# Kernel optimization log

Hardware: AMD Instinct MI355X
Metric: run time of the kernel (lower is better)

## Reference

```python
import jax, jax.numpy as jnp
import numpy as np

H, D, K, FF = 8, 512, 64, 64  # n_head, feature_dim, key_feature_dim, dim_feedforward
L, B = 512, 32
LN_EPS = 1e-5


def _l2norm(x, eps=1e-12):
    # torch F.normalize: x / max(||x||, eps)
    n = jnp.sqrt(jnp.sum(x * x, axis=-1, keepdims=True))
    return x / jnp.maximum(n, eps)


def _layernorm(x, g, b, eps=LN_EPS):
    m = jnp.mean(x, axis=-1, keepdims=True)
    v = jnp.mean((x - m) ** 2, axis=-1, keepdims=True)
    return (x - m) * jax.lax.rsqrt(v + eps) * g + b


def setup_inputs() -> dict:
    key0 = jax.random.key(0)
    ks = jax.random.split(key0, 13)
    n = jax.random.normal
    s_kq = float(np.sqrt(2.0 / K))
    s_v = float(np.sqrt(2.0 / D))
    return {
        "query": n(ks[0], (L, B, D), jnp.float32),
        "key": n(ks[1], (L, B, D), jnp.float32),
        "value": n(ks[2], (L, B, D), jnp.float32),
        "WK": n(ks[3], (H, K, D), jnp.float32) * s_kq,
        "WQ": n(ks[4], (H, K, D), jnp.float32) * s_kq,
        "WV": n(ks[5], (H, D, D), jnp.float32) * s_v,
        "Wt": n(ks[6], (H, D, D), jnp.float32) * 0.04,  # trans_conv (default kaiming-ish scale)
        "W1": n(ks[7], (H, FF, D), jnp.float32) * 0.04,
        "b1": jnp.zeros((H, FF), jnp.float32),
        "W2": n(ks[8], (H, D, FF), jnp.float32) * 0.1,
        "b2": jnp.zeros((H, D), jnp.float32),
        "ln_g": jnp.ones((H, D), jnp.float32),
        "ln_b": jnp.zeros((H, D), jnp.float32),
    }


def reference(query, key, value, WK, WQ, WV, Wt, W1, b1, W2, b2, ln_g, ln_b):
    # query/key/value: [L, B, D]; per-head weights stacked on leading H axis.
    Lq, Bb, Dd = query.shape
    Hh = WK.shape[0]

    # per-head cosine-normalized Q/K projections: [H, B, L, K]
    wq = _l2norm(jnp.einsum('lbd,hkd->hblk', query, WQ))
    wk = _l2norm(jnp.einsum('lbd,hkd->hblk', key, WK))

    # attention scores [H, B, Lq, Lk], temp = 1
    dot = jnp.einsum('hbqc,hbkc->hbqk', wq, wk)
    aff = jax.nn.softmax(dot, axis=-1)
    # custom renorm: divide by column sums over the QUERY axis
    aff = aff / (1e-9 + jnp.sum(aff, axis=2, keepdims=True))

    wv = jnp.einsum('lbd,hed->hble', value, WV)        # [H, B, Lk, D]
    out = jnp.einsum('hbqk,hbke->hbqe', aff, wv)       # [H, B, Lq, D]
    out = jnp.transpose(out, (0, 2, 1, 3))             # [H, L, B, D]

    # residual-style trans_conv(query - out) -> relu
    o = jax.nn.relu(jnp.einsum('hlbd,hed->hlbe', query[None] - out, Wt))

    # TransNonlinear FFN (dropout = identity at eval)
    hff = jax.nn.relu(jnp.einsum('hlbd,hfd->hlbf', o, W1) + b1[:, None, None, :])
    s2 = jnp.einsum('hlbf,hdf->hlbd', hff, W2) + b2[:, None, None, :]
    x = _layernorm(o + s2, ln_g[:, None, None, :], ln_b[:, None, None, :])

    # concat heads on last dim, head 0 first: [L, B, H*D]
    return jnp.transpose(x, (1, 2, 0, 3)).reshape(Lq, Bb, Hh * Dd)
```

## Files before the change

### kernel.cpp

```cpp
#include <hip/hip_runtime.h>
#include <stdint.h>

#define HH 8
#define DDIM 512
#define KHEAD 64
#define FFD 64
#define LLEN 512
#define BBATCH 32
#define NTOK 16384

typedef unsigned short u16;
typedef __attribute__((ext_vector_type(8))) __bf16 bf16x8;
typedef __attribute__((ext_vector_type(4))) float f32x4;

__device__ __forceinline__ float bf2f(u16 u) {
    union { uint32_t i; float f; } v; v.i = ((uint32_t)u) << 16; return v.f;
}
__device__ __forceinline__ u16 f2bf(float f) {
    union { uint32_t i; float f; } v; v.f = f;
    return (u16)((v.i + 0x7FFFu + ((v.i >> 16) & 1u)) >> 16);
}

__device__ __forceinline__ void gload16(const void* g, void* l) {
    __builtin_amdgcn_global_load_lds(
        (const __attribute__((address_space(1))) void*)g,
        (__attribute__((address_space(3))) void*)l, 16, 0, 0);
}

struct ConvJob { const float* s; u16* d; int n4; };
struct ConvJobs { ConvJob j[6]; int nj; };

__global__ __launch_bounds__(256) void conv_multi(ConvJobs jobs) {
    for (int k = 0; k < jobs.nj; ++k) {
        const float* s = jobs.j[k].s;
        u16* d = jobs.j[k].d;
        const int n4 = jobs.j[k].n4;
        for (long i = (long)blockIdx.x * 256 + threadIdx.x; i < n4;
             i += (long)gridDim.x * 256) {
            float4 v = ((const float4*)s)[i];
            ushort4 o;
            o.x = f2bf(v.x); o.y = f2bf(v.y); o.z = f2bf(v.z); o.w = f2bf(v.w);
            ((ushort4*)d)[i] = o;
        }
    }
}

enum { M_PLAIN = 0, M_WQK = 1, M_SUBAUX = 2, M_RELU = 3, M_ADDAUX = 4, M_SCALECOL = 5 };

template<int BM, int BN, int MODE, int ZMAP, int SWAPXY>
__global__ __launch_bounds__(256) void mgemm(
    const u16* __restrict__ A, const u16* __restrict__ B, u16* __restrict__ C,
    int Kd, int lda, int ldb, int ldc,
    long Ash, long Asb, long Bsh, long Bsb, long Csh, long Csb, int nB2,
    const float* __restrict__ bias, int biasN,
    const void* __restrict__ auxp, long auxsh, long auxsb, int auxld)
{
    constexpr int WC = (BN == 128) ? 2 : 1;
    constexpr int WR = 4 / WC;
    constexpr int WTM = BM / WR;
    constexpr int WTN = BN / WC;
    constexpr int MF = WTM / 16;
    constexpr int NF = WTN / 16;
    constexpr int NCA = (BM * 64) / 4096;
    constexpr int NCB = (BN * 64) / 4096;
    __shared__ u16 As[2][BM * 32];
    __shared__ u16 Bs[2][BN * 32];

    const int z = blockIdx.z;
    int h2, b2;
    if (ZMAP == 0)      { h2 = z / nB2;      b2 = z % nB2; }
    else if (ZMAP == 1) { h2 = z & 7;        b2 = z >> 3; }
    else                { h2 = (z >> 3) & 7; b2 = ((z >> 6) << 3) | (z & 7); }
    const u16* Ab = A + h2 * Ash + b2 * Asb;
    const u16* Bb = B + h2 * Bsh + b2 * Bsb;
    const int bx = SWAPXY ? blockIdx.y : blockIdx.x;
    const int by = SWAPXY ? blockIdx.x : blockIdx.y;
    const int m0 = bx * BM, n0 = by * BN;
    const int t = threadIdx.x;
    const int lane = t & 63;
    const int w = t >> 6;
    const int wr = w / WC, wc = w % WC;
    const int tb = t * 16;
    const int wb = (t & 192) * 16;

    f32x4 acc[MF][NF];
    #pragma unroll
    for (int m = 0; m < MF; ++m)
        #pragma unroll
        for (int n = 0; n < NF; ++n)
            #pragma unroll
            for (int i = 0; i < 4; ++i) acc[m][n][i] = 0.f;

    const int ko = (lane >> 4) * 16;

    auto stage = [&](int buf, int k0) {
        #pragma unroll
        for (int c = 0; c < NCA; ++c) {
            const int byte = c * 4096 + tb;
            const int row = byte >> 6;
            gload16((const char*)(Ab + (long)(m0 + row) * lda + k0) + (byte & 63),
                    (char*)As[buf] + c * 4096 + wb);
        }
        #pragma unroll
        for (int c = 0; c < NCB; ++c) {
            const int byte = c * 4096 + tb;
            const int row = byte >> 6;
            gload16((const char*)(Bb + (long)(n0 + row) * ldb + k0) + (byte & 63),
                    (char*)Bs[buf] + c * 4096 + wb);
        }
    };

    stage(0, 0);
    __syncthreads();
    int cur = 0;
    const int nsteps = Kd >> 5;
    for (int s = 0; s < nsteps; ++s) {
        if (s + 1 < nsteps) stage(cur ^ 1, (s + 1) << 5);
        bf16x8 af[MF], bfr[NF];
        #pragma unroll
        for (int m = 0; m < MF; ++m)
            af[m] = *(const bf16x8*)((const char*)As[cur] + (wr * WTM + m * 16 + (lane & 15)) * 64 + ko);
        #pragma unroll
        for (int n = 0; n < NF; ++n)
            bfr[n] = *(const bf16x8*)((const char*)Bs[cur] + (wc * WTN + n * 16 + (lane & 15)) * 64 + ko);
        #pragma unroll
        for (int m = 0; m < MF; ++m)
            #pragma unroll
            for (int n = 0; n < NF; ++n)
                acc[m][n] = __builtin_amdgcn_mfma_f32_16x16x32_bf16(af[m], bfr[n], acc[m][n], 0, 0, 0);
        __syncthreads();
        cur ^= 1;
    }

    const int lr = (lane >> 4) * 4;
    const int lc = lane & 15;

    if constexpr (MODE == M_WQK) {
        const int h = (n0 + wc * WTN) >> 6;
        #pragma unroll
        for (int m = 0; m < MF; ++m) {
            #pragma unroll
            for (int i = 0; i < 4; ++i) {
                float s = 0.f;
                #pragma unroll
                for (int n = 0; n < NF; ++n) { const float v = acc[m][n][i]; s += v * v; }
                s += __shfl_xor(s, 1); s += __shfl_xor(s, 2);
                s += __shfl_xor(s, 4); s += __shfl_xor(s, 8);
                const float inv = 1.0f / fmaxf(sqrtf(s), 1e-12f);
                const int r = m0 + wr * WTM + m * 16 + lr + i;
                const int l = r >> 5, bq = r & 31;
                const int sw = (l & 7) << 3;
                u16* rowp = C + (((long)(h * BBATCH + bq) * LLEN + l) * KHEAD);
                #pragma unroll
                for (int n = 0; n < NF; ++n)
                    rowp[(lc + n * 16) ^ sw] = f2bf(acc[m][n][i] * inv);
            }
        }
    } else {
        const long cof = h2 * Csh + b2 * Csb;
        #pragma unroll
        for (int m = 0; m < MF; ++m) {
            #pragma unroll
            for (int i = 0; i < 4; ++i) {
                const int r = m0 + wr * WTM + m * 16 + lr + i;
                #pragma unroll
                for (int n = 0; n < NF; ++n) {
                    const int c = n0 + wc * WTN + n * 16 + lc;
                    float v = acc[m][n][i];
                    if (MODE == M_SUBAUX) {
                        const u16* q = (const u16*)auxp;
                        v = bf2f(q[auxsh * h2 + auxsb * b2 + (long)r * auxld + c]) - v;
                    } else if (MODE == M_RELU) {
                        if (bias) v += bias[h2 * biasN + c];
                        v = fmaxf(v, 0.0f);
                    } else if (MODE == M_ADDAUX) {
                        v += bias[h2 * biasN + c];
                        const u16* ax = (const u16*)auxp;
                        v += bf2f(ax[auxsh * h2 + auxsb * b2 + (long)r * auxld + c]);
                    } else if (MODE == M_SCALECOL) {
                        const float* cs = (const float*)auxp + auxsh * h2 + auxsb * b2;
                        v *= 1.0f / (1e-9f + cs[c]);
                    }
                    C[cof + (long)r * ldc + c] = f2bf(v);
                }
            }
        }
    }
}

__device__ __forceinline__ void xcd_decode(int wgid, int& qt, int& b, int& h) {
    const int r = wgid & 7;
    const int inner = wgid >> 3;
    qt = inner & 7;
    h = (inner >> 3) & 7;
    b = ((inner >> 6) << 3) | r;
}

__global__ __launch_bounds__(256) void attn_mfma(
    const u16* __restrict__ wq, const u16* __restrict__ wk,
    u16* __restrict__ P, float* __restrict__ colsum)
{
    __shared__ u16 qs[64 * 64];
    __shared__ u16 ks[512 * 64];
    __shared__ float smax[4][64];
    __shared__ float ssum[4][64];

    int qt, b, h;
    xcd_decode(blockIdx.x, qt, b, h);
    const long hb = h * BBATCH + b;
    const int t = threadIdx.x;
    const int lane = t & 63, w = t >> 6;
    const int wb = (t & 192) * 16;

    const char* qg = (const char*)(wq + (hb * LLEN + qt * 64) * KHEAD);
    const char* kg = (const char*)(wk + hb * LLEN * KHEAD);
    #pragma unroll
    for (int c = 0; c < 2; ++c)
        gload16(qg + c * 4096 + t * 16, (char*)qs + c * 4096 + wb);
    #pragma unroll
    for (int c = 0; c < 16; ++c)
        gload16(kg + c * 4096 + t * 16, (char*)ks + c * 4096 + wb);
    __syncthreads();

    const int l15 = lane & 15;
    const int g = lane >> 4;
    const int swz = (lane & 7) << 4;

    f32x4 acc[4][8];
    #pragma unroll
    for (int m = 0; m < 4; ++m)
        #pragma unroll
        for (int n = 0; n < 8; ++n)
            #pragma unroll
            for (int i = 0; i < 4; ++i) acc[m][n][i] = 0.f;

    #pragma unroll
    for (int kk = 0; kk < 2; ++kk) {
        bf16x8 af[4];
        #pragma unroll
        for (int m = 0; m < 4; ++m) {
            const int row = m * 16 + l15;
            af[m] = *(const bf16x8*)((const char*)qs + row * 128 + ((g * 16 + kk * 64) ^ swz));
        }
        #pragma unroll
        for (int n = 0; n < 8; ++n) {
            const int row = (w * 8 + n) * 16 + l15;
            const bf16x8 bfr = *(const bf16x8*)((const char*)ks + row * 128 + ((g * 16 + kk * 64) ^ swz));
            #pragma unroll
            for (int m = 0; m < 4; ++m)
                acc[m][n] = __builtin_amdgcn_mfma_f32_16x16x32_bf16(af[m], bfr, acc[m][n], 0, 0, 0);
        }
    }

    float rmax[4][4];
    #pragma unroll
    for (int m = 0; m < 4; ++m)
        #pragma unroll
        for (int i = 0; i < 4; ++i) {
            float mx = acc[m][0][i];
            #pragma unroll
            for (int n = 1; n < 8; ++n) mx = fmaxf(mx, acc[m][n][i]);
            mx = fmaxf(mx, __shfl_xor(mx, 1));
            mx = fmaxf(mx, __shfl_xor(mx, 2));
            mx = fmaxf(mx, __shfl_xor(mx, 4));
            mx = fmaxf(mx, __shfl_xor(mx, 8));
            if (l15 == 0) smax[w][m * 16 + g * 4 + i] = mx;
        }
    __syncthreads();
    #pragma unroll
    for (int m = 0; m < 4; ++m)
        #pragma unroll
        for (int i = 0; i < 4; ++i) {
            const int r = m * 16 + g * 4 + i;
            rmax[m][i] = fmaxf(fmaxf(smax[0][r], smax[1][r]),
                               fmaxf(smax[2][r], smax[3][r]));
        }
    float rinv[4][4];
    #pragma unroll
    for (int m = 0; m < 4; ++m)
        #pragma unroll
        for (int i = 0; i < 4; ++i) {
            float s = 0.f;
            #pragma unroll
            for (int n = 0; n < 8; ++n) {
                acc[m][n][i] = __expf(acc[m][n][i] - rmax[m][i]);
                s += acc[m][n][i];
            }
            s += __shfl_xor(s, 1); s += __shfl_xor(s, 2);
            s += __shfl_xor(s, 4); s += __shfl_xor(s, 8);
            if (l15 == 0) ssum[w][m * 16 + g * 4 + i] = s;
        }
    __syncthreads();
    #pragma unroll
    for (int m = 0; m < 4; ++m)
        #pragma unroll
        for (int i = 0; i < 4; ++i) {
            const int r = m * 16 + g * 4 + i;
            rinv[m][i] = 1.0f / (ssum[0][r] + ssum[1][r] + ssum[2][r] + ssum[3][r]);
        }

    u16* Pb = P + (hb * LLEN + qt * 64) * LLEN + w * 128;
    float cs[8];
    #pragma unroll
    for (int n = 0; n < 8; ++n) cs[n] = 0.f;
    #pragma unroll
    for (int m = 0; m < 4; ++m)
        #pragma unroll
        for (int i = 0; i < 4; ++i) {
            const int r = m * 16 + g * 4 + i;
            u16* pr = Pb + (long)r * LLEN + l15;
            const float iv = rinv[m][i];
            #pragma unroll
            for (int n = 0; n < 8; ++n) {
                const float p = acc[m][n][i] * iv;
                pr[n * 16] = f2bf(p);
                cs[n] += p;
            }
        }
    #pragma unroll
    for (int n = 0; n < 8; ++n) {
        cs[n] += __shfl_xor(cs[n], 16);
        cs[n] += __shfl_xor(cs[n], 32);
    }
    if (lane < 16) {
        float* cb = colsum + hb * 512 + w * 128 + lane;
        #pragma unroll
        for (int n = 0; n < 8; ++n) atomicAdd(&cb[n * 16], cs[n]);
    }
}

__global__ __launch_bounds__(256) void ffn2_ln(
    const u16* __restrict__ hff, const u16* __restrict__ W2bf,
    const float* __restrict__ b2, const u16* __restrict__ o,
    const float* __restrict__ lng, const float* __restrict__ lnb,
    float* __restrict__ out)
{
    __shared__ u16 W2s[512 * 64];
    __shared__ u16 hs[32 * 64];
    __shared__ float redS[4][32];
    __shared__ float redQ[4][32];

    const int h = blockIdx.z;
    const int m0 = blockIdx.x * 32;
    const int t = threadIdx.x;
    const int lane = t & 63, w = t >> 6;
    const int l15 = lane & 15, g = lane >> 4;
    const int wb = (t & 192) * 16;

    const char* w2g = (const char*)W2bf + (long)h * 65536;
    #pragma unroll
    for (int c = 0; c < 16; ++c) {
        const int idx = c * 4096 + t * 16;
        const int row = idx >> 7;
        const int g0 = (idx >> 4) & 7;
        gload16(w2g + row * 128 + ((g0 ^ (row & 7)) << 4),
                (char*)W2s + c * 4096 + wb);
    }
    {
        const int idx = t * 16;
        const int row = idx >> 7;
        const int g0 = (idx >> 4) & 7;
        gload16((const char*)(hff + ((long)h * NTOK + m0) * FFD) +
                    row * 128 + ((g0 ^ (row & 7)) << 4),
                (char*)hs + wb);
    }
    __syncthreads();

    f32x4 acc[2][8];
    #pragma unroll
    for (int m = 0; m < 2; ++m)
        #pragma unroll
        for (int n = 0; n < 8; ++n)
            #pragma unroll
            for (int i = 0; i < 4; ++i) acc[m][n][i] = 0.f;

    #pragma unroll
    for (int kk = 0; kk < 2; ++kk) {
        bf16x8 af[2];
        #pragma unroll
        for (int m = 0; m < 2; ++m) {
            const int row = m * 16 + l15;
            af[m] = *(const bf16x8*)((const char*)hs + row * 128 +
                                     (((kk * 4 + g) ^ (row & 7)) << 4));
        }
        #pragma unroll
        for (int n = 0; n < 8; ++n) {
            const int e = w * 128 + n * 16 + l15;
            const bf16x8 bfr = *(const bf16x8*)((const char*)W2s + e * 128 +
                                                (((kk * 4 + g) ^ (e & 7)) << 4));
            #pragma unroll
            for (int m = 0; m < 2; ++m)
                acc[m][n] = __builtin_amdgcn_mfma_f32_16x16x32_bf16(af[m], bfr, acc[m][n], 0, 0, 0);
        }
    }

    float b2v[8], gv[8], bv[8];
    #pragma unroll
    for (int n = 0; n < 8; ++n) {
        const int c = w * 128 + n * 16 + l15;
        b2v[n] = b2[h * DDIM + c];
        gv[n] = lng[h * DDIM + c];
        bv[n] = lnb[h * DDIM + c];
    }
    const u16* ob = o + ((long)h * NTOK + m0) * DDIM;
    #pragma unroll
    for (int m = 0; m < 2; ++m)
        #pragma unroll
        for (int i = 0; i < 4; ++i) {
            const int row = m * 16 + g * 4 + i;
            float s = 0.f, q = 0.f;
            #pragma unroll
            for (int n = 0; n < 8; ++n) {
                const int c = w * 128 + n * 16 + l15;
                const float v = acc[m][n][i] + b2v[n] + bf2f(ob[(long)row * DDIM + c]);
                acc[m][n][i] = v;
                s += v; q += v * v;
            }
            s += __shfl_xor(s, 1); q += __shfl_xor(q, 1);
            s += __shfl_xor(s, 2); q += __shfl_xor(q, 2);
            s += __shfl_xor(s, 4); q += __shfl_xor(q, 4);
            s += __shfl_xor(s, 8); q += __shfl_xor(q, 8);
            if (l15 == 0) { redS[w][row] = s; redQ[w][row] = q; }
        }
    __syncthreads();

    #pragma unroll
    for (int m = 0; m < 2; ++m)
        #pragma unroll
        for (int i = 0; i < 4; ++i) {
            const int row = m * 16 + g * 4 + i;
            const float s = redS[0][row] + redS[1][row] + redS[2][row] + redS[3][row];
            const float q = redQ[0][row] + redQ[1][row] + redQ[2][row] + redQ[3][row];
            const float mu = s * (1.0f / 512.0f);
            const float var = q * (1.0f / 512.0f) - mu * mu;
            const float rs = rsqrtf(var + 1e-5f);
            const int tok = m0 + row;
            const int b = tok >> 9, l = tok & 511;
            float* op = out + ((long)(l * BBATCH + b)) * (HH * DDIM) + h * DDIM;
            #pragma unroll
            for (int n = 0; n < 8; ++n) {
                const int c = w * 128 + n * 16 + l15;
                op[c] = (acc[m][n][i] - mu) * rs * gv[n] + bv[n];
            }
        }
}

extern "C" void kernel_launch(void* const* d_in, const int* in_sizes, int n_in,
                              void* d_out, int out_size, void* d_ws, size_t ws_size,
                              hipStream_t stream) {
    const float* query = (const float*)d_in[0];
    const float* key   = (const float*)d_in[1];
    const float* value = (const float*)d_in[2];
    const float* WK = (const float*)d_in[3];
    const float* WQ = (const float*)d_in[4];
    const float* WV = (const float*)d_in[5];
    const float* Wt = (const float*)d_in[6];
    const float* W1 = (const float*)d_in[7];
    const float* b1 = (const float*)d_in[8];
    const float* W2 = (const float*)d_in[9];
    const float* b2 = (const float*)d_in[10];
    const float* lng = (const float*)d_in[11];
    const float* lnb = (const float*)d_in[12];

    char* ws = (char*)d_ws;
    u16* kbf  = (u16*)(ws);
    u16* WQbf = (u16*)(ws + 16777216);
    u16* WKbf = (u16*)(ws + 17301504);
    u16* P    = (u16*)(ws);
    u16* vbf  = (u16*)(ws + 134217728);
    u16* WVbf = (u16*)(ws + 150994944);
    u16* o    = (u16*)(ws + 134217728);
    float* colsum = (float*)(ws + 268435456);
    u16* qbf  = (u16*)(ws + 268959744);
    u16* hff  = qbf;
    u16* wq   = (u16*)(ws + 285736960);
    u16* wk   = (u16*)(ws + 302514176);
    u16* Wtbf = (u16*)(ws + 285736960);
    u16* W1bf = (u16*)(ws + 289931264);
    u16* W2bf = (u16*)(ws + 290455552);
    u16* qmo = (u16*)d_out;
    u16* wvT = (u16*)((char*)d_out + 134217728);

    if (ws_size < 319291392u) return;

    hipMemsetAsync(colsum, 0, 524288, stream);
    const dim3 blk(256);

    {
        ConvJobs J;
        J.j[0] = { query, qbf, 2097152 };
        J.j[1] = { key,   kbf, 2097152 };
        J.j[2] = { value, vbf, 2097152 };
        J.j[3] = { WQ, WQbf, 65536 };
        J.j[4] = { WK, WKbf, 65536 };
        J.j[5] = { WV, WVbf, 524288 };
        J.nj = 6;
        conv_multi<<<dim3(2048), blk, 0, stream>>>(J);
    }

    mgemm<128, 128, M_WQK, 0, 1><<<dim3(4, 128, 1), blk, 0, stream>>>(
        qbf, WQbf, wq, 512, 512, 512, 0,
        0, 0, 0, 0, 0, 0, 1, nullptr, 0, nullptr, 0, 0, 0);
    mgemm<128, 128, M_WQK, 0, 1><<<dim3(4, 128, 1), blk, 0, stream>>>(
        kbf, WKbf, wk, 512, 512, 512, 0,
        0, 0, 0, 0, 0, 0, 1, nullptr, 0, nullptr, 0, 0, 0);

    attn_mfma<<<dim3(2048), blk, 0, stream>>>(wq, wk, P, colsum);

    {
        ConvJobs J;
        J.j[0] = { Wt, Wtbf, 524288 };
        J.j[1] = { W1, W1bf, 65536 };
        J.j[2] = { W2, W2bf, 65536 };
        J.nj = 3;
        conv_multi<<<dim3(1024), blk, 0, stream>>>(J);
    }

    mgemm<128, 128, M_SCALECOL, 2, 0><<<dim3(4, 4, 256), blk, 0, stream>>>(
        WVbf, vbf, wvT, 512, 512, BBATCH * DDIM, 512,
        (long)DDIM * DDIM, 0, 0, DDIM,
        (long)BBATCH * DDIM * LLEN, (long)DDIM * LLEN, 32,
        nullptr, 0, colsum, (long)BBATCH * 512, 512, 0);

    mgemm<128, 128, M_SUBAUX, 1, 0><<<dim3(4, 4, 256), blk, 0, stream>>>(
        P, wvT, qmo, 512, 512, 512, 512,
        (long)BBATCH * LLEN * LLEN, (long)LLEN * LLEN,
        (long)BBATCH * DDIM * LLEN, (long)DDIM * LLEN,
        (long)BBATCH * LLEN * DDIM, (long)LLEN * DDIM, 32,
        nullptr, 0, qbf, 0, DDIM, BBATCH * DDIM);

    mgemm<128, 128, M_RELU, 0, 1><<<dim3(4, 128, 8), blk, 0, stream>>>(
        qmo, Wtbf, o, 512, 512, 512, 512,
        (long)NTOK * DDIM, 0, (long)DDIM * DDIM, 0,
        (long)NTOK * DDIM, 0, 1, nullptr, 512, nullptr, 0, 0, 0);

    mgemm<128, 64, M_RELU, 0, 0><<<dim3(128, 1, 8), blk, 0, stream>>>(
        o, W1bf, hff, 512, 512, 512, 64,
        (long)NTOK * DDIM, 0, (long)FFD * DDIM, 0,
        (long)NTOK * FFD, 0, 1, b1, 64, nullptr, 0, 0, 0);

    ffn2_ln<<<dim3(512, 1, 8), blk, 0, stream>>>(hff, W2bf, b2, o, lng, lnb,
                                                 (float*)d_out);
}
```

Before: 766.2 us.

## Add 256x256-tile 512-thread GEMM kernel for the three large batched GEMMs

Result: faster. 746.4 us, median of 2 (-2.6%).

```diff
diff --git a/kernel.cpp b/kernel.cpp
--- a/kernel.cpp
+++ b/kernel.cpp
@@ -46,6 +46,138 @@
 }
 
 enum { M_PLAIN = 0, M_WQK = 1, M_SUBAUX = 2, M_RELU = 3, M_ADDAUX = 4, M_SCALECOL = 5 };
+
+template<int MODE, int ZMAP, int SWAPXY>
+__global__ __launch_bounds__(512) void mgemm256(
+    const u16* __restrict__ A, const u16* __restrict__ B, u16* __restrict__ C,
+    int Kd, int lda, int ldb, int ldc,
+    long Ash, long Asb, long Bsh, long Bsb, long Csh, long Csb, int nB2,
+    const float* __restrict__ bias, int biasN,
+    const void* __restrict__ auxp, long auxsh, long auxsb, int auxld)
+{
+    __shared__ u16 As[2][256 * 64];
+    __shared__ u16 Bs[2][256 * 64];
+
+    const int z = blockIdx.z;
+    int h2, b2;
+    if (ZMAP == 0)      { h2 = z / nB2;      b2 = z % nB2; }
+    else if (ZMAP == 1) { h2 = z & 7;        b2 = z >> 3; }
+    else                { h2 = (z >> 3) & 7; b2 = ((z >> 6) << 3) | (z & 7); }
+    const int bx = SWAPXY ? blockIdx.y : blockIdx.x;
+    const int by = SWAPXY ? blockIdx.x : blockIdx.y;
+    const int m0 = bx * 256, n0 = by * 256;
+    const u16* Ab = A + h2 * Ash + b2 * Asb + (long)m0 * lda;
+    const u16* Bb = B + h2 * Bsh + b2 * Bsb + (long)n0 * ldb;
+
+    const int t = threadIdx.x;
+    const int lane = t & 63;
+    const int w = t >> 6;
+    const int wm = w >> 2;
+    const int wn = w & 3;
+    const int l15 = lane & 15;
+    const int g = lane >> 4;
+
+    f32x4 acc[8][4];
+    #pragma unroll
+    for (int mf = 0; mf < 8; ++mf)
+        #pragma unroll
+        for (int nf = 0; nf < 4; ++nf)
+            #pragma unroll
+            for (int i = 0; i < 4; ++i) acc[mf][nf][i] = 0.f;
+
+    auto stageT = [&](int buf, int k0) {
+        #pragma unroll
+        for (int c = 0; c < 4; ++c) {
+            const int idx = c * 8192 + t * 16;
+            const int row = idx >> 7;
+            const int g0 = (idx >> 4) & 7;
+            gload16((const char*)(Ab + (long)row * lda + k0) + ((g0 ^ (row & 7)) << 4),
+                    (char*)As[buf] + c * 8192 + w * 1024);
+        }
+        #pragma unroll
+        for (int c = 0; c < 4; ++c) {
+            const int idx = c * 8192 + t * 16;
+            const int row = idx >> 7;
+            const int g0 = (idx >> 4) & 7;
+            gload16((const char*)(Bb + (long)row * ldb + k0) + ((g0 ^ (row & 7)) << 4),
+                    (char*)Bs[buf] + c * 8192 + w * 1024);
+        }
+    };
+
+    stageT(0, 0);
+    const int nt = Kd >> 6;
+    for (int T = 0; T < nt; ++T) {
+        asm volatile("s_waitcnt vmcnt(0)" ::: "memory");
+        __builtin_amdgcn_sched_barrier(0);
+        __builtin_amdgcn_s_barrier();
+        __builtin_amdgcn_sched_barrier(0);
+        if (T + 1 < nt) stageT((T + 1) & 1, (T + 1) << 6);
+
+        const char* Abase = (const char*)As[T & 1];
+        const char* Bbase = (const char*)Bs[T & 1];
+        #pragma unroll
+        for (int q = 0; q < 4; ++q) {
+            const int mh = q >> 1, nh = q & 1;
+            bf16x8 af[4][2], bfv[2][2];
+            #pragma unroll
+            for (int mf = 0; mf < 4; ++mf) {
+                const int row = wm * 128 + (mh * 4 + mf) * 16 + l15;
+                #pragma unroll
+                for (int kk = 0; kk < 2; ++kk)
+                    af[mf][kk] = *(const bf16x8*)(Abase + row * 128 +
+                                      (((kk * 4 + g) ^ (row & 7)) << 4));
+            }
+            #pragma unroll
+            for (int nf = 0; nf < 2; ++nf) {
+                const int row = wn * 64 + (nh * 2 + nf) * 16 + l15;
+                #pragma unroll
+                for (int kk = 0; kk < 2; ++kk)
+                    bfv[nf][kk] = *(const bf16x8*)(Bbase + row * 128 +
+                                      (((kk * 4 + g) ^ (row & 7)) << 4));
+            }
+            __builtin_amdgcn_s_setprio(1);
+            #pragma unroll
+            for (int kk = 0; kk < 2; ++kk)
+                #pragma unroll
+                for (int mf = 0; mf < 4; ++mf)
+                    #pragma unroll
+                    for (int nf = 0; nf < 2; ++nf)
+                        acc[mh * 4 + mf][nh * 2 + nf] =
+                            __builtin_amdgcn_mfma_f32_16x16x32_bf16(
+                                af[mf][kk], bfv[nf][kk],
+                                acc[mh * 4 + mf][nh * 2 + nf], 0, 0, 0);
+            __builtin_amdgcn_s_setprio(0);
+            __builtin_amdgcn_sched_barrier(0);
+        }
+    }
+
+    const int lr = g * 4;
+    const int lc = l15;
+    const long cof = h2 * Csh + b2 * Csb;
+    #pragma unroll
+    for (int mf = 0; mf < 8; ++mf) {
+        #pragma unroll
+        for (int i = 0; i < 4; ++i) {
+            const int r = m0 + wm * 128 + mf * 16 + lr + i;
+            #pragma unroll
+            for (int nf = 0; nf < 4; ++nf) {
+                const int c = n0 + wn * 64 + nf * 16 + lc;
+                float v = acc[mf][nf][i];
+                if (MODE == M_SUBAUX) {
+                    const u16* q = (const u16*)auxp;
+                    v = bf2f(q[auxsh * h2 + auxsb * b2 + (long)r * auxld + c]) - v;
+                } else if (MODE == M_RELU) {
+                    if (bias) v += bias[h2 * biasN + c];
+                    v = fmaxf(v, 0.0f);
+                } else if (MODE == M_SCALECOL) {
+                    const float* cs = (const float*)auxp + auxsh * h2 + auxsb * b2;
+                    v *= 1.0f / (1e-9f + cs[c]);
+                }
+                C[cof + (long)r * ldc + c] = f2bf(v);
+            }
+        }
+    }
+}
 
 template<int BM, int BN, int MODE, int ZMAP, int SWAPXY>
 __global__ __launch_bounds__(256) void mgemm(
@@ -516,20 +648,20 @@
         conv_multi<<<dim3(1024), blk, 0, stream>>>(J);
     }
 
-    mgemm<128, 128, M_SCALECOL, 2, 0><<<dim3(4, 4, 256), blk, 0, stream>>>(
+    mgemm256<M_SCALECOL, 2, 0><<<dim3(2, 2, 256), dim3(512), 0, stream>>>(
         WVbf, vbf, wvT, 512, 512, BBATCH * DDIM, 512,
         (long)DDIM * DDIM, 0, 0, DDIM,
         (long)BBATCH * DDIM * LLEN, (long)DDIM * LLEN, 32,
         nullptr, 0, colsum, (long)BBATCH * 512, 512, 0);
 
-    mgemm<128, 128, M_SUBAUX, 1, 0><<<dim3(4, 4, 256), blk, 0, stream>>>(
+    mgemm256<M_SUBAUX, 1, 0><<<dim3(2, 2, 256), dim3(512), 0, stream>>>(
         P, wvT, qmo, 512, 512, 512, 512,
         (long)BBATCH * LLEN * LLEN, (long)LLEN * LLEN,
         (long)BBATCH * DDIM * LLEN, (long)DDIM * LLEN,
         (long)BBATCH * LLEN * DDIM, (long)LLEN * DDIM, 32,
         nullptr, 0, qbf, 0, DDIM, BBATCH * DDIM);
 
-    mgemm<128, 128, M_RELU, 0, 1><<<dim3(4, 128, 8), blk, 0, stream>>>(
+    mgemm256<M_RELU, 0, 1><<<dim3(2, 64, 8), dim3(512), 0, stream>>>(
         qmo, Wtbf, o, 512, 512, 512, 512,
         (long)NTOK * DDIM, 0, (long)DDIM * DDIM, 0,
         (long)NTOK * DDIM, 0, 1, nullptr, 512, nullptr, 0, 0, 0);
```
